# Optimization experiments

Measured on AMD Instinct MI355X. Metric: run time of the kernel, lower is better.

Reference implementation:

```python
import jax, jax.numpy as jnp
import numpy as np

B, N, E, H = 16, 577, 1024, 16          # batch, tokens (1 cls + 24x24 patches), embed, heads
HD = E // H
LORA_E, LORA_R = 4, 16                   # LoRA experts, rank
AD_E, AD_D = 4, 64                       # adapter experts, bottleneck
FF = 4 * E


def setup_inputs() -> dict:
    key = jax.random.key(0)
    ks = jax.random.split(key, 12)
    p = lambda i, shape: jax.random.normal(ks[i], shape, dtype=jnp.float32) * 0.02
    return {
        "tokens": jax.random.normal(ks[0], (B, N, E), dtype=jnp.float32),
        "ln1_g": jnp.ones((E,), jnp.float32), "ln1_b": jnp.zeros((E,), jnp.float32),
        "qkv_w": p(1, (3 * E, E)), "qkv_b": jnp.zeros((3 * E,), jnp.float32),
        "proj_w": p(2, (E, E)), "proj_b": jnp.zeros((E,), jnp.float32),
        "lora_gate_w": p(3, (LORA_E, E)),
        "lora_A": p(4, (LORA_E, LORA_R, E)),
        "lora_B": p(5, (LORA_E, 3 * E, LORA_R)),
        "ln2_g": jnp.ones((E,), jnp.float32), "ln2_b": jnp.zeros((E,), jnp.float32),
        "fc1_w": p(6, (FF, E)), "fc1_b": jnp.zeros((FF,), jnp.float32),
        "fc2_w": p(7, (E, FF)), "fc2_b": jnp.zeros((E,), jnp.float32),
        "ad_gate_w": p(8, (AD_E, E)),
        "ad_down_w": p(9, (AD_E, AD_D, E)), "ad_down_b": jnp.zeros((AD_E, AD_D), jnp.float32),
        "ad_up_w": p(10, (AD_E, E, AD_D)), "ad_up_b": jnp.zeros((AD_E, E), jnp.float32),
    }


def _ln(x, g, b):
    m = x.mean(-1, keepdims=True)
    v = ((x - m) ** 2).mean(-1, keepdims=True)
    return (x - m) * jax.lax.rsqrt(v + 1e-6) * g + b


def reference(tokens, ln1_g, ln1_b, qkv_w, qkv_b, proj_w, proj_b,
              lora_gate_w, lora_A, lora_B, ln2_g, ln2_b,
              fc1_w, fc1_b, fc2_w, fc2_b,
              ad_gate_w, ad_down_w, ad_down_b, ad_up_w, ad_up_b):
    # ---- attention with MoE-LoRA delta on fused QKV ----
    normed = _ln(tokens, ln1_g, ln1_b)                      # [B,N,E]
    qkv = normed @ qkv_w.T + qkv_b                          # [B,N,3E]
    gates = jax.nn.softmax(normed @ lora_gate_w.T, axis=-1)  # [B,N,X]
    h = jnp.einsum('bnd,xrd->bnxr', normed, lora_A)         # low-rank down
    delta = jnp.einsum('bnxr,bnx,xor->bno', h, gates, lora_B)  # gate-weighted up
    qkv = (qkv + delta).reshape(B, N, 3, H, HD).transpose(2, 0, 3, 1, 4)
    q, k, v = qkv[0], qkv[1], qkv[2]                        # [B,H,N,hd]
    scores = jnp.einsum('bhqd,bhkd->bhqk', q, k) * (HD ** -0.5)
    probs = jax.nn.softmax(scores, axis=-1)
    ctx = jnp.einsum('bhqk,bhkd->bhqd', probs, v)
    ctx = ctx.transpose(0, 2, 1, 3).reshape(B, N, E)
    tokens = tokens + (ctx @ proj_w.T + proj_b)
    # ---- MLP + MoE adapter branch (shared norm2 input) ----
    mlp_in = _ln(tokens, ln2_g, ln2_b)
    mlp_out = jax.nn.gelu(mlp_in @ fc1_w.T + fc1_b, approximate=False) @ fc2_w.T + fc2_b
    ag = jax.nn.softmax(mlp_in @ ad_gate_w.T, axis=-1)       # [B,N,Xa]
    ah = jax.nn.gelu(jnp.einsum('bnd,xhd->bnxh', mlp_in, ad_down_w) + ad_down_b,
                     approximate=False)
    ad_out = (jnp.einsum('bnxh,bnx,xoh->bno', ah, ag, ad_up_w)
              + jnp.einsum('bnx,xo->bno', ag, ad_up_b))
    return tokens + mlp_out + ad_out
```

## Files before the change

kernel.cpp:

```cpp
#include <hip/hip_runtime.h>
#include <math.h>

#define TOK 9232
#define EMB 1024
#define NQKV 3072
#define FFD 4096
#define NSEQ 577

typedef __bf16 bf16x8 __attribute__((ext_vector_type(8)));
typedef float f32x4 __attribute__((ext_vector_type(4)));
typedef unsigned short ushort8 __attribute__((ext_vector_type(8)));
typedef unsigned short ushort4v __attribute__((ext_vector_type(4)));

typedef __attribute__((address_space(3))) unsigned int lds_u32_t;
typedef const __attribute__((address_space(1))) unsigned int glob_u32_t;

__device__ __forceinline__ void async16(void* lds, const void* g) {
    __builtin_amdgcn_global_load_lds((glob_u32_t*)g, (lds_u32_t*)lds, 16, 0, 0);
}

__device__ __forceinline__ unsigned short f2bf(float f) {
    unsigned int u = __builtin_bit_cast(unsigned int, f);
    u = (u + 0x7fffu + ((u >> 16) & 1u)) >> 16;
    return (unsigned short)u;
}
__device__ __forceinline__ float bf2f(unsigned short s) {
    unsigned int u = ((unsigned int)s) << 16;
    return __builtin_bit_cast(float, u);
}
__device__ __forceinline__ float gelu_exact(float x) {
    return 0.5f * x * (1.0f + erff(x * 0.70710678118654752f));
}

__global__ void k_pack_all(const float* __restrict__ s_qkv, const float* __restrict__ s_proj,
                           const float* __restrict__ s_fc1, const float* __restrict__ s_fc2,
                           const float* __restrict__ s_la,  const float* __restrict__ s_ad,
                           unsigned short* __restrict__ d_qkv, unsigned short* __restrict__ d_proj,
                           unsigned short* __restrict__ d_fc1, unsigned short* __restrict__ d_fc2,
                           unsigned short* __restrict__ d_la,  unsigned short* __restrict__ d_ad) {
    int stride = gridDim.x * 256;
    for (int i4 = blockIdx.x * 256 + threadIdx.x; i4 < 3227648; i4 += stride) {
        const float* s; unsigned short* d; int local;
        if (i4 < 786432)       { s = s_qkv;  d = d_qkv;  local = i4; }
        else if (i4 < 1048576) { s = s_proj; d = d_proj; local = i4 - 786432; }
        else if (i4 < 2097152) { s = s_fc1;  d = d_fc1;  local = i4 - 1048576; }
        else if (i4 < 3145728) { s = s_fc2;  d = d_fc2;  local = i4 - 2097152; }
        else if (i4 < 3162112) { s = s_la;   d = d_la;   local = i4 - 3145728; }
        else                   { s = s_ad;   d = d_ad;   local = i4 - 3162112; }
        float4 v = ((const float4*)s)[local];
        ushort4v o;
        o[0] = f2bf(v.x); o[1] = f2bf(v.y); o[2] = f2bf(v.z); o[3] = f2bf(v.w);
        ((ushort4v*)d)[local] = o;
    }
}
__global__ void k_pack_bcat(const float* __restrict__ Bw, unsigned short* __restrict__ out) {
    int i = blockIdx.x * 256 + threadIdx.x;
    if (i >= 3072 * 64) return;
    int o = i >> 6, j = i & 63, x = j >> 4, r = j & 15;
    out[o * 64 + j] = f2bf(Bw[x * 3072 * 16 + o * 16 + r]);
}
__global__ void k_pack_u(const float* __restrict__ Uw, unsigned short* __restrict__ out) {
    int i = blockIdx.x * 256 + threadIdx.x;
    if (i >= 1024 * 256) return;
    int o = i >> 8, j = i & 255, x = j >> 6, h = j & 63;
    out[o * 256 + j] = f2bf(Uw[x * 65536 + o * 64 + h]);
}

template<bool FC2I>
__global__ __launch_bounds__(256) void k_ln_gates(const float* __restrict__ x,
                                                  const float* __restrict__ g,
                                                  const float* __restrict__ b,
                                                  const float* __restrict__ gw,
                                                  unsigned short* __restrict__ out,
                                                  float* __restrict__ gates,
                                                  const float* __restrict__ fc2b,
                                                  const float* __restrict__ upb,
                                                  float* __restrict__ out2) {
    int t = blockIdx.x;
    int tid = threadIdx.x;
    const float* xp = x + (size_t)t * EMB;
    float4 v = ((const float4*)xp)[tid];
    float s = v.x + v.y + v.z + v.w;
    float sq = v.x * v.x + v.y * v.y + v.z * v.z + v.w * v.w;
    #pragma unroll
    for (int off = 32; off > 0; off >>= 1) {
        s += __shfl_down(s, off);
        sq += __shfl_down(sq, off);
    }
    __shared__ float red[8];
    if ((tid & 63) == 0) { red[tid >> 6] = s; red[(tid >> 6) + 4] = sq; }
    __syncthreads();
    float S = red[0] + red[1] + red[2] + red[3];
    float SQ = red[4] + red[5] + red[6] + red[7];
    float mean = S * (1.0f / EMB);
    float var = SQ * (1.0f / EMB) - mean * mean;
    float rstd = rsqrtf(var + 1e-6f);
    float4 gv = ((const float4*)g)[tid];
    float4 bv = ((const float4*)b)[tid];
    float n0 = (v.x - mean) * rstd * gv.x + bv.x;
    float n1 = (v.y - mean) * rstd * gv.y + bv.y;
    float n2 = (v.z - mean) * rstd * gv.z + bv.z;
    float n3 = (v.w - mean) * rstd * gv.w + bv.w;
    ushort4v o;
    o[0] = f2bf(n0); o[1] = f2bf(n1); o[2] = f2bf(n2); o[3] = f2bf(n3);
    ((ushort4v*)(out + (size_t)t * EMB))[tid] = o;
    float p[4];
    #pragma unroll
    for (int xx = 0; xx < 4; ++xx) {
        float4 gr = ((const float4*)(gw + xx * EMB))[tid];
        p[xx] = n0 * gr.x + n1 * gr.y + n2 * gr.z + n3 * gr.w;
    }
    #pragma unroll
    for (int off = 32; off > 0; off >>= 1) {
        #pragma unroll
        for (int xx = 0; xx < 4; ++xx) p[xx] += __shfl_down(p[xx], off);
    }
    __shared__ float red2[4][4];
    __shared__ float agb[4];
    if ((tid & 63) == 0) {
        #pragma unroll
        for (int xx = 0; xx < 4; ++xx) red2[tid >> 6][xx] = p[xx];
    }
    __syncthreads();
    if (tid == 0) {
        float l[4];
        #pragma unroll
        for (int xx = 0; xx < 4; ++xx) l[xx] = red2[0][xx] + red2[1][xx] + red2[2][xx] + red2[3][xx];
        float m = fmaxf(fmaxf(l[0], l[1]), fmaxf(l[2], l[3]));
        float e[4], ssum = 0.f;
        #pragma unroll
        for (int xx = 0; xx < 4; ++xx) { e[xx] = expf(l[xx] - m); ssum += e[xx]; }
        float inv = 1.0f / ssum;
        #pragma unroll
        for (int xx = 0; xx < 4; ++xx) {
            float gg = e[xx] * inv;
            gates[t * 4 + xx] = gg;
            if (FC2I) agb[xx] = gg;
        }
    }
    if (FC2I) {
        __syncthreads();
        float g0 = agb[0], g1 = agb[1], g2 = agb[2], g3 = agb[3];
        float4 b0 = ((const float4*)(upb + 0 * EMB))[tid];
        float4 b1 = ((const float4*)(upb + 1 * EMB))[tid];
        float4 b2 = ((const float4*)(upb + 2 * EMB))[tid];
        float4 b3 = ((const float4*)(upb + 3 * EMB))[tid];
        float4 fb = ((const float4*)fc2b)[tid];
        float4 r;
        r.x = v.x + fb.x + g0 * b0.x + g1 * b1.x + g2 * b2.x + g3 * b3.x;
        r.y = v.y + fb.y + g0 * b0.y + g1 * b1.y + g2 * b2.y + g3 * b3.y;
        r.z = v.z + fb.z + g0 * b0.z + g1 * b1.z + g2 * b2.z + g3 * b3.z;
        r.w = v.w + fb.w + g0 * b0.w + g1 * b1.w + g2 * b2.w + g3 * b3.w;
        ((float4*)(out2 + (size_t)t * EMB))[tid] = r;
    }
}

#define BAR __builtin_amdgcn_s_barrier()

template<bool GELU, bool BF16OUT, int GG, int MF, int NF, int CN>
__global__ __launch_bounds__(256) void k_gemm(
    const unsigned short* __restrict__ A, int lda,
    const unsigned short* __restrict__ W, int ldw, int K1,
    int M, int N,
    const unsigned short* __restrict__ A2, const unsigned short* __restrict__ W2, int K2,
    const float* __restrict__ bias, const float* __restrict__ resid,
    const float* __restrict__ aux,
    void* __restrict__ Cout, int ldc, int gy)
{
    constexpr int CA = MF * 4;
    constexpr int CB = NF * 4;
    constexpr int CT = CA + CB;
    constexpr int CPW = CT / 4;
    constexpr int BUFB = CT * 1024;
    __shared__ __attribute__((aligned(16))) char Sbuf[2 * BUFB];

    int tid = threadIdx.x;
    int nwg = gridDim.x, orig = blockIdx.x;
    int xcd = orig & 7, lid = orig >> 3;
    int q = nwg >> 3, r = nwg & 7;
    int wg = (xcd < r ? xcd * (q + 1) : r * (q + 1) + (xcd - r) * q) + lid;
    int nmt = nwg / gy;
    int ni = wg % CN;
    int tmp = wg / CN;
    int mt = tmp % nmt;
    int nt = (tmp / nmt) * CN + ni;
    int bm = mt * (MF * 32);
    int bn = nt * (NF * 32);

    int l = tid & 63, w = tid >> 6;
    int wr = w >> 1, wc = w & 1;
    int lr = l & 15;
    int sslot = (((l & 7) ^ (l >> 3)) << 3);

    int KT1 = K1 >> 6, KT2 = K2 >> 6;
    int KT = KT1 + KT2;

    const unsigned short* A2s = A2 ? A2 : A;
    const unsigned short* W2s = W2 ? W2 : W;
    int K2s = A2 ? K2 : lda;

    const unsigned short* sp1[CPW];
    const unsigned short* sp2[CPW];
    int ldsu[CPW];
    #pragma unroll
    for (int j = 0; j < CPW; ++j) {
        int c = w * CPW + j;
        ldsu[j] = c << 10;
        if (c < CA) {
            int rw = bm + c * 8 + (l >> 3); if (rw > M - 1) rw = M - 1;
            sp1[j] = A + (size_t)rw * lda + sslot;
            sp2[j] = A2s + (size_t)rw * K2s + sslot;
        } else {
            int rw = bn + (c - CA) * 8 + (l >> 3); if (rw > N - 1) rw = N - 1;
            sp1[j] = W + (size_t)rw * ldw + sslot;
            sp2[j] = W2s + (size_t)rw * K2s + sslot;
        }
    }

    int offA[MF][2], offB[NF][2];
    #pragma unroll
    for (int m = 0; m < MF; ++m)
        #pragma unroll
        for (int ks = 0; ks < 2; ++ks) {
            int rw = wr * (MF * 16) + m * 16 + lr;
            int g = ks * 4 + (l >> 4);
            offA[m][ks] = (rw << 7) + ((g ^ (rw & 7)) << 4);
        }
    #pragma unroll
    for (int n = 0; n < NF; ++n)
        #pragma unroll
        for (int ks = 0; ks < 2; ++ks) {
            int rw = wc * (NF * 16) + n * 16 + lr;
            int g = ks * 4 + (l >> 4);
            offB[n][ks] = (CA << 10) + (rw << 7) + ((g ^ (rw & 7)) << 4);
        }

    f32x4 acc[MF][NF];
    #pragma unroll
    for (int m = 0; m < MF; ++m)
        #pragma unroll
        for (int n = 0; n < NF; ++n) acc[m][n] = (f32x4){0.f, 0.f, 0.f, 0.f};

    auto stage = [&](int ss, int bb) {
        char* db = Sbuf + bb * BUFB;
        if (ss < KT1) {
            int ko = ss << 6;
            #pragma unroll
            for (int j = 0; j < CPW; ++j) async16(db + ldsu[j], sp1[j] + ko);
        } else {
            int ko = (ss - KT1) << 6;
            #pragma unroll
            for (int j = 0; j < CPW; ++j) async16(db + ldsu[j], sp2[j] + ko);
        }
    };

    stage(0, 0);

    #pragma unroll 1
    for (int t = 0; t < KT; ++t) {
        asm volatile("s_waitcnt vmcnt(0)" ::: "memory");
        BAR;
        __builtin_amdgcn_sched_barrier(0);
        int s = t + 1; if (s >= KT) s = 0;
        stage(s, (t + 1) & 1);
        const char* base = Sbuf + (t & 1) * BUFB;
        bf16x8 af[MF][2], bfr[NF][2];
        #pragma unroll
        for (int m = 0; m < MF; ++m)
            #pragma unroll
            for (int ks = 0; ks < 2; ++ks) af[m][ks] = *(const bf16x8*)(base + offA[m][ks]);
        #pragma unroll
        for (int n = 0; n < NF; ++n)
            #pragma unroll
            for (int ks = 0; ks < 2; ++ks) bfr[n][ks] = *(const bf16x8*)(base + offB[n][ks]);
        __builtin_amdgcn_s_setprio(1);
        #pragma unroll
        for (int m = 0; m < MF; ++m)
            #pragma unroll
            for (int n = 0; n < NF; ++n)
                #pragma unroll
                for (int ks = 0; ks < 2; ++ks)
                    acc[m][n] = __builtin_amdgcn_mfma_f32_16x16x32_bf16(af[m][ks], bfr[n][ks], acc[m][n], 0, 0, 0);
        __builtin_amdgcn_s_setprio(0);
    }

    int rbase = bm + wr * (MF * 16);
    int cbase = bn + wc * (NF * 16);
    #pragma unroll
    for (int n = 0; n < NF; ++n) {
        int col = cbase + n * 16 + lr;
        if (col >= N) continue;
        float bv = bias ? bias[col] : 0.0f;
        #pragma unroll
        for (int m = 0; m < MF; ++m) {
            #pragma unroll
            for (int rr = 0; rr < 4; ++rr) {
                int row = rbase + m * 16 + (l >> 4) * 4 + rr;
                if (row >= M) continue;
                float c = acc[m][n][rr] + bv;
                if (GELU) c = gelu_exact(c);
                if (GG > 0) c *= aux[row * 4 + col / (GG > 0 ? GG : 1)];
                if (resid) c += resid[(size_t)row * ldc + col];
                if (BF16OUT) ((unsigned short*)Cout)[(size_t)row * ldc + col] = f2bf(c);
                else ((float*)Cout)[(size_t)row * ldc + col] = c;
            }
        }
    }
}

__global__ __launch_bounds__(256) void k_attn(const unsigned short* __restrict__ qkv,
                                              unsigned short* __restrict__ ctx) {
    int bh = blockIdx.x;
    int qt = blockIdx.y;
    int b = bh >> 4, h = bh & 15;
    int tid = threadIdx.x;
    int l = tid & 63;
    int w = tid >> 6;
    int lr = l & 15;
    int lk = (l >> 4) * 8;

    __shared__ unsigned short Qs[64][72];
    __shared__ unsigned short Ks[64][72];
    __shared__ unsigned short Vt[64][72];
    __shared__ unsigned short Ps[64][72];

    const size_t base = (size_t)b * NSEQ * NQKV + (size_t)h * 64;
    int q0 = qt * 64;

    {
        int row = tid >> 2, ds = (tid & 3) * 16;
        int qrow = q0 + row;
        if (qrow < NSEQ) {
            const unsigned short* src = qkv + base + (size_t)qrow * NQKV + ds;
            *(ushort8*)&Qs[row][ds] = *(const ushort8*)src;
            *(ushort8*)&Qs[row][ds + 8] = *(const ushort8*)(src + 8);
        } else {
            ushort8 z = {};
            *(ushort8*)&Qs[row][ds] = z;
            *(ushort8*)&Qs[row][ds + 8] = z;
        }
    }

    float m_run[4], l_run[4];
    f32x4 o[4];
    #pragma unroll
    for (int r = 0; r < 4; ++r) { m_run[r] = -1e30f; l_run[r] = 0.0f; }
    #pragma unroll
    for (int n = 0; n < 4; ++n) o[n] = (f32x4){0.f, 0.f, 0.f, 0.f};

    for (int kt = 0; kt < 10; ++kt) {
        __syncthreads();
        {
            int row = tid >> 2, ds = (tid & 3) * 16;
            int key = kt * 64 + row;
            if (key < NSEQ) {
                const unsigned short* ksrc = qkv + base + (size_t)key * NQKV + 1024 + ds;
                *(ushort8*)&Ks[row][ds] = *(const ushort8*)ksrc;
                *(ushort8*)&Ks[row][ds + 8] = *(const ushort8*)(ksrc + 8);
                const unsigned short* vsrc = qkv + base + (size_t)key * NQKV + 2048 + ds;
                #pragma unroll
                for (int j = 0; j < 16; ++j) Vt[ds + j][row] = vsrc[j];
            } else {
                ushort8 z = {};
                *(ushort8*)&Ks[row][ds] = z;
                *(ushort8*)&Ks[row][ds + 8] = z;
                #pragma unroll
                for (int j = 0; j < 16; ++j) Vt[ds + j][row] = 0;
            }
        }
        __syncthreads();

        f32x4 s[4];
        #pragma unroll
        for (int n = 0; n < 4; ++n) s[n] = (f32x4){0.f, 0.f, 0.f, 0.f};
        #pragma unroll
        for (int ks = 0; ks < 2; ++ks) {
            bf16x8 qa = *(const bf16x8*)&Qs[w * 16 + lr][ks * 32 + lk];
            #pragma unroll
            for (int n = 0; n < 4; ++n) {
                bf16x8 kb = *(const bf16x8*)&Ks[n * 16 + lr][ks * 32 + lk];
                s[n] = __builtin_amdgcn_mfma_f32_16x16x32_bf16(qa, kb, s[n], 0, 0, 0);
            }
        }
        #pragma unroll
        for (int n = 0; n < 4; ++n) {
            #pragma unroll
            for (int r = 0; r < 4; ++r) s[n][r] *= 0.125f;
        }
        #pragma unroll
        for (int n = 0; n < 4; ++n) {
            int col = kt * 64 + n * 16 + lr;
            if (col >= NSEQ) {
                #pragma unroll
                for (int r = 0; r < 4; ++r) s[n][r] = -1e30f;
            }
        }
        float tmax[4];
        #pragma unroll
        for (int r = 0; r < 4; ++r)
            tmax[r] = fmaxf(fmaxf(s[0][r], s[1][r]), fmaxf(s[2][r], s[3][r]));
        #pragma unroll
        for (int off = 1; off < 16; off <<= 1) {
            #pragma unroll
            for (int r = 0; r < 4; ++r) tmax[r] = fmaxf(tmax[r], __shfl_xor(tmax[r], off));
        }
        float alpha[4], rs[4];
        #pragma unroll
        for (int r = 0; r < 4; ++r) {
            float mn = fmaxf(m_run[r], tmax[r]);
            alpha[r] = __expf(m_run[r] - mn);
            m_run[r] = mn;
            rs[r] = 0.0f;
        }
        #pragma unroll
        for (int n = 0; n < 4; ++n) {
            #pragma unroll
            for (int r = 0; r < 4; ++r) {
                float p = __expf(s[n][r] - m_run[r]);
                s[n][r] = p;
                rs[r] += p;
            }
        }
        #pragma unroll
        for (int off = 1; off < 16; off <<= 1) {
            #pragma unroll
            for (int r = 0; r < 4; ++r) rs[r] += __shfl_xor(rs[r], off);
        }
        #pragma unroll
        for (int r = 0; r < 4; ++r) l_run[r] = l_run[r] * alpha[r] + rs[r];
        #pragma unroll
        for (int n = 0; n < 4; ++n) {
            #pragma unroll
            for (int r = 0; r < 4; ++r) o[n][r] *= alpha[r];
        }
        #pragma unroll
        for (int n = 0; n < 4; ++n) {
            #pragma unroll
            for (int r = 0; r < 4; ++r)
                Ps[w * 16 + (l >> 4) * 4 + r][n * 16 + lr] = f2bf(s[n][r]);
        }
        __syncthreads();
        #pragma unroll
        for (int ks = 0; ks < 2; ++ks) {
            bf16x8 pa = *(const bf16x8*)&Ps[w * 16 + lr][ks * 32 + lk];
            #pragma unroll
            for (int n = 0; n < 4; ++n) {
                bf16x8 vb = *(const bf16x8*)&Vt[n * 16 + lr][ks * 32 + lk];
                o[n] = __builtin_amdgcn_mfma_f32_16x16x32_bf16(pa, vb, o[n], 0, 0, 0);
            }
        }
    }
    #pragma unroll
    for (int r = 0; r < 4; ++r) {
        int qrow = q0 + w * 16 + (l >> 4) * 4 + r;
        if (qrow < NSEQ) {
            float inv = (l_run[r] > 0.f) ? 1.0f / l_run[r] : 0.0f;
            #pragma unroll
            for (int n = 0; n < 4; ++n)
                ctx[((size_t)b * NSEQ + qrow) * EMB + h * 64 + n * 16 + lr] = f2bf(o[n][r] * inv);
        }
    }
}

extern "C" void kernel_launch(void* const* d_in, const int* in_sizes, int n_in,
                              void* d_out, int out_size, void* d_ws, size_t ws_size,
                              hipStream_t stream) {
    const float* tokens      = (const float*)d_in[0];
    const float* ln1_g       = (const float*)d_in[1];
    const float* ln1_b       = (const float*)d_in[2];
    const float* qkv_w       = (const float*)d_in[3];
    const float* qkv_b       = (const float*)d_in[4];
    const float* proj_w      = (const float*)d_in[5];
    const float* proj_b      = (const float*)d_in[6];
    const float* lora_gate_w = (const float*)d_in[7];
    const float* lora_A      = (const float*)d_in[8];
    const float* lora_B      = (const float*)d_in[9];
    const float* ln2_g       = (const float*)d_in[10];
    const float* ln2_b       = (const float*)d_in[11];
    const float* fc1_w       = (const float*)d_in[12];
    const float* fc1_b       = (const float*)d_in[13];
    const float* fc2_w       = (const float*)d_in[14];
    const float* fc2_b       = (const float*)d_in[15];
    const float* ad_gate_w   = (const float*)d_in[16];
    const float* ad_down_w   = (const float*)d_in[17];
    const float* ad_down_b   = (const float*)d_in[18];
    const float* ad_up_w     = (const float*)d_in[19];
    const float* ad_up_b     = (const float*)d_in[20];

    char* ws = (char*)d_ws;
    size_t off = 0;
    auto alloc = [&](size_t bytes) -> void* {
        void* p = ws + off;
        off += (bytes + 255) & ~(size_t)255;
        return p;
    };

    unsigned short* w_qkv  = (unsigned short*)alloc((size_t)NQKV * EMB * 2);
    unsigned short* w_proj = (unsigned short*)alloc((size_t)EMB * EMB * 2);
    unsigned short* w_fc1  = (unsigned short*)alloc((size_t)FFD * EMB * 2);
    unsigned short* w_fc2  = (unsigned short*)alloc((size_t)EMB * FFD * 2);
    unsigned short* w_acat = (unsigned short*)alloc((size_t)64 * EMB * 2);
    unsigned short* w_bcat = (unsigned short*)alloc((size_t)NQKV * 64 * 2);
    unsigned short* w_dcat = (unsigned short*)alloc((size_t)256 * EMB * 2);
    unsigned short* w_u    = (unsigned short*)alloc((size_t)EMB * 256 * 2);

    unsigned short* u1 = (unsigned short*)alloc((size_t)TOK * EMB * 2);
    unsigned short* u2 = (unsigned short*)alloc((size_t)TOK * EMB * 2);
    unsigned short* u3 = (unsigned short*)alloc((size_t)TOK * FFD * 2);
    float* tok2  = (float*)alloc((size_t)TOK * EMB * 4);
    unsigned short* hw  = (unsigned short*)alloc((size_t)TOK * 64 * 2);
    unsigned short* ahw = (unsigned short*)alloc((size_t)TOK * 256 * 2);
    float* gates = (float*)alloc((size_t)TOK * 4 * 4);
    float* ag    = (float*)alloc((size_t)TOK * 4 * 4);

    unsigned short* normed = u1;
    unsigned short* mlpin  = u1;
    unsigned short* ctx    = u2;
    unsigned short* qkv    = u3;
    unsigned short* h1     = u3;

    k_pack_all<<<2048, 256, 0, stream>>>(qkv_w, proj_w, fc1_w, fc2_w, lora_A, ad_down_w,
                                         w_qkv, w_proj, w_fc1, w_fc2, w_acat, w_dcat);
    k_pack_bcat<<<(NQKV * 64 + 255) / 256, 256, 0, stream>>>(lora_B, w_bcat);
    k_pack_u<<<(EMB * 256 + 255) / 256, 256, 0, stream>>>(ad_up_w, w_u);

    k_ln_gates<false><<<TOK, 256, 0, stream>>>(tokens, ln1_g, ln1_b, lora_gate_w,
                                               normed, gates, nullptr, nullptr, nullptr);
    k_gemm<false, true, 16, 2, 2, 1><<<145, 256, 0, stream>>>(
        normed, EMB, w_acat, EMB, EMB, TOK, 64,
        nullptr, nullptr, 0, nullptr, nullptr, gates, hw, 64, 1);
    k_gemm<false, true, 0, 4, 2, 8><<<73 * 48, 256, 0, stream>>>(
        normed, EMB, w_qkv, EMB, EMB, TOK, NQKV,
        hw, w_bcat, 64, qkv_b, nullptr, nullptr, qkv, NQKV, 48);
    k_attn<<<dim3(256, 10), 256, 0, stream>>>(qkv, ctx);
    k_gemm<false, false, 0, 4, 2, 8><<<73 * 16, 256, 0, stream>>>(
        ctx, EMB, w_proj, EMB, EMB, TOK, EMB,
        nullptr, nullptr, 0, proj_b, tokens, nullptr, tok2, EMB, 16);
    k_ln_gates<true><<<TOK, 256, 0, stream>>>(tok2, ln2_g, ln2_b, ad_gate_w,
                                              mlpin, ag, fc2_b, ad_up_b, (float*)d_out);
    k_gemm<true, true, 64, 2, 2, 4><<<145 * 4, 256, 0, stream>>>(
        mlpin, EMB, w_dcat, EMB, EMB, TOK, 256,
        nullptr, nullptr, 0, ad_down_b, nullptr, ag, ahw, 256, 4);
    k_gemm<true, true, 0, 4, 2, 8><<<73 * 64, 256, 0, stream>>>(
        mlpin, EMB, w_fc1, EMB, EMB, TOK, FFD,
        nullptr, nullptr, 0, fc1_b, nullptr, nullptr, h1, FFD, 64);
    k_gemm<false, false, 0, 4, 2, 8><<<73 * 16, 256, 0, stream>>>(
        h1, FFD, w_fc2, FFD, FFD, TOK, EMB,
        ahw, w_u, 256, nullptr, (const float*)d_out, nullptr, (float*)d_out, EMB, 16);
}
```

Before: 634.9 us.

## Add 256x256-tile 8-wave pipelined GEMM kernel for fc1

Introduces a new GEMM kernel with 256x256 output tiles, 512 threads, an XOR-swizzled double-buffered LDS layout and an interleaved stage/MFMA schedule with explicit vmcnt waits and setprio. The fc1 projection now uses it instead of the 128x128-style generic kernel, aiming for more data reuse per loaded tile and better overlap of global loads with MFMA work. In exchange it needs large LDS and register use at occupancy 1, and wastes more padded rows in the last M tile since 9232 is not a multiple of 256.

```diff
diff --git a/kernel.cpp b/kernel.cpp
--- a/kernel.cpp
+++ b/kernel.cpp
@@ -303,6 +303,167 @@
                 if (resid) c += resid[(size_t)row * ldc + col];
                 if (BF16OUT) ((unsigned short*)Cout)[(size_t)row * ldc + col] = f2bf(c);
                 else ((float*)Cout)[(size_t)row * ldc + col] = c;
+            }
+        }
+    }
+}
+
+__device__ __forceinline__ void stage_half256(
+    const unsigned short* __restrict__ src, int ldk, int kc,
+    int row0, int rmax, char* lds_half, int w, int l)
+{
+    #pragma unroll
+    for (int j = 0; j < 2; ++j) {
+        int P = j * 8192 + w * 1024 + l * 16;
+        int row = P >> 7;
+        int slot = ((P >> 4) & 7) ^ (row & 7);
+        int r = row0 + row; if (r > rmax) r = rmax;
+        async16(lds_half + j * 8192 + w * 1024,
+                src + (size_t)r * ldk + kc + slot * 8);
+    }
+}
+
+__device__ __forceinline__ bf16x8 lds_frag256(const char* tile, int row, int c0) {
+    int byte = (row << 7) + (c0 << 1);
+    byte ^= (row & 7) << 4;
+    return *(const bf16x8*)(tile + byte);
+}
+
+#define STAGE256_A(s, ht, Pb) do {                                         \
+    int s_ = (s); if (s_ >= KT) s_ = 0;                                    \
+    stage_half256(A, K, s_ << 6, bm + (ht) * 128, M - 1,                   \
+                  (char*)SA + (Pb) * 32768 + (ht) * 16384, w, l);          \
+} while (0)
+
+#define STAGE256_B(s, ht, Pb) do {                                         \
+    int s_ = (s); if (s_ >= KT) s_ = 0;                                    \
+    stage_half256(W, K, s_ << 6, bn + (ht) * 128, N - 1,                   \
+                  (char*)SB + (Pb) * 32768 + (ht) * 16384, w, l);          \
+} while (0)
+
+#define LDA256(Pb, MH)                                                     \
+    _Pragma("unroll")                                                      \
+    for (int f_ = 0; f_ < 4; ++f_)                                         \
+        _Pragma("unroll")                                                  \
+        for (int ks_ = 0; ks_ < 2; ++ks_)                                  \
+            a[f_][ks_] = lds_frag256((const char*)SA + (Pb) * 32768,       \
+                wm * 128 + (MH) * 64 + f_ * 16 + lr, ks_ * 32 + lk8);
+
+#define LDB256(Pb, NH, BREG)                                               \
+    _Pragma("unroll")                                                      \
+    for (int n_ = 0; n_ < 2; ++n_)                                         \
+        _Pragma("unroll")                                                  \
+        for (int ks_ = 0; ks_ < 2; ++ks_)                                  \
+            BREG[n_][ks_] = lds_frag256((const char*)SB + (Pb) * 32768,    \
+                wn * 64 + (NH) * 32 + n_ * 16 + lr, ks_ * 32 + lk8);
+
+#define MFMA256(MH, NH, BREG)                                              \
+    __builtin_amdgcn_s_setprio(1);                                         \
+    _Pragma("unroll")                                                      \
+    for (int f_ = 0; f_ < 4; ++f_)                                         \
+        _Pragma("unroll")                                                  \
+        for (int n_ = 0; n_ < 2; ++n_)                                     \
+            _Pragma("unroll")                                              \
+            for (int ks_ = 0; ks_ < 2; ++ks_)                              \
+                acc[(MH) * 4 + f_][(NH) * 2 + n_] =                        \
+                    __builtin_amdgcn_mfma_f32_16x16x32_bf16(               \
+                        a[f_][ks_], BREG[n_][ks_],                         \
+                        acc[(MH) * 4 + f_][(NH) * 2 + n_], 0, 0, 0);       \
+    __builtin_amdgcn_s_setprio(0);
+
+#define VMCNT4_256 asm volatile("s_waitcnt vmcnt(4)" ::: "memory")
+
+template<bool GELU, bool BF16OUT>
+__global__ __launch_bounds__(512, 1) void k_gemm256(
+    const unsigned short* __restrict__ A, const unsigned short* __restrict__ W,
+    int M, int N, int K,
+    const float* __restrict__ bias,
+    void* __restrict__ Cout, int ldc, int NT)
+{
+    __shared__ __attribute__((aligned(16))) unsigned short SA[2][256][64];
+    __shared__ __attribute__((aligned(16))) unsigned short SB[2][256][64];
+
+    int tid = threadIdx.x;
+    int l = tid & 63, w = tid >> 6;
+    int wm = w >> 2, wn = w & 3;
+    int lr = l & 15, lk8 = (l >> 4) * 8;
+
+    int nwg = gridDim.x, orig = blockIdx.x;
+    int xcd = orig & 7, lid = orig >> 3;
+    int q = nwg >> 3, r = nwg & 7;
+    int wg = (xcd < r ? xcd * (q + 1) : r * (q + 1) + (xcd - r) * q) + lid;
+    int bm = (wg / NT) * 256;
+    int bn = (wg % NT) * 256;
+
+    int KT = K >> 6;
+
+    f32x4 acc[8][4];
+    #pragma unroll
+    for (int i = 0; i < 8; ++i)
+        #pragma unroll
+        for (int j = 0; j < 4; ++j) acc[i][j] = (f32x4){0.f, 0.f, 0.f, 0.f};
+
+    STAGE256_A(0, 0, 0); STAGE256_A(0, 1, 0);
+    STAGE256_B(0, 0, 0); STAGE256_B(0, 1, 0);
+    STAGE256_B(1, 0, 1); STAGE256_B(1, 1, 1);
+    VMCNT4_256;
+    BAR;
+
+    bf16x8 a[4][2], b0[2][2], b1[2][2];
+
+    int SI = KT >> 1;
+    #pragma unroll 1
+    for (int i = 0; i < SI; ++i) {
+        int t0 = i * 2;
+        LDA256(0, 0); LDB256(0, 0, b0);
+        STAGE256_A(t0 + 1, 0, 1);
+        BAR; MFMA256(0, 0, b0); BAR;
+
+        LDB256(0, 1, b1);
+        STAGE256_A(t0 + 1, 1, 1);
+        BAR; MFMA256(0, 1, b1); BAR;
+
+        LDA256(0, 1);
+        STAGE256_B(t0 + 2, 0, 0);
+        BAR; MFMA256(1, 0, b0); BAR;
+
+        STAGE256_B(t0 + 2, 1, 0);
+        VMCNT4_256;
+        BAR; MFMA256(1, 1, b1); BAR;
+
+        LDA256(1, 0); LDB256(1, 0, b0);
+        STAGE256_A(t0 + 2, 0, 0);
+        BAR; MFMA256(0, 0, b0); BAR;
+
+        LDB256(1, 1, b1);
+        STAGE256_A(t0 + 2, 1, 0);
+        BAR; MFMA256(0, 1, b1); BAR;
+
+        LDA256(1, 1);
+        STAGE256_B(t0 + 3, 0, 1);
+        BAR; MFMA256(1, 0, b0); BAR;
+
+        STAGE256_B(t0 + 3, 1, 1);
+        VMCNT4_256;
+        BAR; MFMA256(1, 1, b1); BAR;
+    }
+
+    #pragma unroll
+    for (int G = 0; G < 4; ++G) {
+        int col = bn + wn * 64 + (G >> 1) * 32 + (G & 1) * 16 + lr;
+        float bv = bias ? bias[col] : 0.0f;
+        #pragma unroll
+        for (int F = 0; F < 8; ++F) {
+            int row0 = bm + wm * 128 + (F >> 2) * 64 + (F & 3) * 16 + (l >> 4) * 4;
+            #pragma unroll
+            for (int rr = 0; rr < 4; ++rr) {
+                int row = row0 + rr;
+                if (row < M) {
+                    float c = acc[F][G][rr] + bv;
+                    if (GELU) c = gelu_exact(c);
+                    if (BF16OUT) ((unsigned short*)Cout)[(size_t)row * ldc + col] = f2bf(c);
+                    else ((float*)Cout)[(size_t)row * ldc + col] = c;
+                }
             }
         }
     }
@@ -541,9 +702,8 @@
     k_gemm<true, true, 64, 2, 2, 4><<<145 * 4, 256, 0, stream>>>(
         mlpin, EMB, w_dcat, EMB, EMB, TOK, 256,
         nullptr, nullptr, 0, ad_down_b, nullptr, ag, ahw, 256, 4);
-    k_gemm<true, true, 0, 4, 2, 8><<<73 * 64, 256, 0, stream>>>(
-        mlpin, EMB, w_fc1, EMB, EMB, TOK, FFD,
-        nullptr, nullptr, 0, fc1_b, nullptr, nullptr, h1, FFD, 64);
+    k_gemm256<true, true><<<37 * 16, 512, 0, stream>>>(
+        mlpin, w_fc1, TOK, FFD, EMB, fc1_b, h1, FFD, 16);
     k_gemm<false, false, 0, 4, 2, 8><<<73 * 16, 256, 0, stream>>>(
         h1, FFD, w_fc2, FFD, FFD, TOK, EMB,
         ahw, w_u, 256, nullptr, (const float*)d_out, nullptr, (float*)d_out, EMB, 16);
```

Measured after the change: 692.8 us. 1.09x slower.

## Halve GEMM K-step to 32 and widen N tiles to 128 columns

Applied to the files above, without the earlier changes.

The GEMM kernel's K-tile shrinks from 64 to 32 elements per stage, with a new LDS row layout and XOR swizzle sized for 64-byte rows. The freed shared memory goes to wider tiles: the big QKV, proj, fc1 and fc2 GEMMs move from 128x64 to 128x128 output tiles, which halves their grid sizes. The aim is more operand reuse per LDS load and fewer global fetches per FLOP. In exchange there are twice as many barrier-synchronised K iterations, each doing less MFMA work, so latency may be harder to hide. More accumulators per thread may also cut occupancy.

```diff
diff --git a/kernel.cpp b/kernel.cpp
--- a/kernel.cpp
+++ b/kernel.cpp
@@ -167,8 +167,8 @@
     const float* __restrict__ aux,
     void* __restrict__ Cout, int ldc, int gy)
 {
-    constexpr int CA = MF * 4;
-    constexpr int CB = NF * 4;
+    constexpr int CA = MF * 2;
+    constexpr int CB = NF * 2;
     constexpr int CT = CA + CB;
     constexpr int CPW = CT / 4;
     constexpr int BUFB = CT * 1024;
@@ -190,9 +190,9 @@
     int l = tid & 63, w = tid >> 6;
     int wr = w >> 1, wc = w & 1;
     int lr = l & 15;
-    int sslot = (((l & 7) ^ (l >> 3)) << 3);
-
-    int KT1 = K1 >> 6, KT2 = K2 >> 6;
+    int sslot = (((l & 3) ^ ((l >> 3) & 3)) << 3);
+
+    int KT1 = K1 >> 5, KT2 = K2 >> 5;
     int KT = KT1 + KT2;
 
     const unsigned short* A2s = A2 ? A2 : A;
@@ -207,33 +207,22 @@
         int c = w * CPW + j;
         ldsu[j] = c << 10;
         if (c < CA) {
-            int rw = bm + c * 8 + (l >> 3); if (rw > M - 1) rw = M - 1;
+            int rw = bm + c * 16 + (l >> 2); if (rw > M - 1) rw = M - 1;
             sp1[j] = A + (size_t)rw * lda + sslot;
             sp2[j] = A2s + (size_t)rw * K2s + sslot;
         } else {
-            int rw = bn + (c - CA) * 8 + (l >> 3); if (rw > N - 1) rw = N - 1;
+            int rw = bn + (c - CA) * 16 + (l >> 2); if (rw > N - 1) rw = N - 1;
             sp1[j] = W + (size_t)rw * ldw + sslot;
             sp2[j] = W2s + (size_t)rw * K2s + sslot;
         }
     }
 
-    int offA[MF][2], offB[NF][2];
-    #pragma unroll
-    for (int m = 0; m < MF; ++m)
-        #pragma unroll
-        for (int ks = 0; ks < 2; ++ks) {
-            int rw = wr * (MF * 16) + m * 16 + lr;
-            int g = ks * 4 + (l >> 4);
-            offA[m][ks] = (rw << 7) + ((g ^ (rw & 7)) << 4);
-        }
-    #pragma unroll
-    for (int n = 0; n < NF; ++n)
-        #pragma unroll
-        for (int ks = 0; ks < 2; ++ks) {
-            int rw = wc * (NF * 16) + n * 16 + lr;
-            int g = ks * 4 + (l >> 4);
-            offB[n][ks] = (CA << 10) + (rw << 7) + ((g ^ (rw & 7)) << 4);
-        }
+    int psl = ((l >> 4) ^ ((lr >> 1) & 3)) << 4;
+    int offA[MF], offB[NF];
+    #pragma unroll
+    for (int m = 0; m < MF; ++m) offA[m] = ((wr * (MF * 16) + m * 16 + lr) << 6) + psl;
+    #pragma unroll
+    for (int n = 0; n < NF; ++n) offB[n] = (CA << 10) + ((wc * (NF * 16) + n * 16 + lr) << 6) + psl;
 
     f32x4 acc[MF][NF];
     #pragma unroll
@@ -244,11 +233,11 @@
     auto stage = [&](int ss, int bb) {
         char* db = Sbuf + bb * BUFB;
         if (ss < KT1) {
-            int ko = ss << 6;
+            int ko = ss << 5;
             #pragma unroll
             for (int j = 0; j < CPW; ++j) async16(db + ldsu[j], sp1[j] + ko);
         } else {
-            int ko = (ss - KT1) << 6;
+            int ko = (ss - KT1) << 5;
             #pragma unroll
             for (int j = 0; j < CPW; ++j) async16(db + ldsu[j], sp2[j] + ko);
         }
@@ -264,23 +253,17 @@
         int s = t + 1; if (s >= KT) s = 0;
         stage(s, (t + 1) & 1);
         const char* base = Sbuf + (t & 1) * BUFB;
-        bf16x8 af[MF][2], bfr[NF][2];
+        bf16x8 af[MF], bfr[NF];
+        #pragma unroll
+        for (int m = 0; m < MF; ++m) af[m] = *(const bf16x8*)(base + offA[m]);
+        #pragma unroll
+        for (int n = 0; n < NF; ++n) bfr[n] = *(const bf16x8*)(base + offB[n]);
+        __builtin_amdgcn_s_setprio(1);
         #pragma unroll
         for (int m = 0; m < MF; ++m)
             #pragma unroll
-            for (int ks = 0; ks < 2; ++ks) af[m][ks] = *(const bf16x8*)(base + offA[m][ks]);
-        #pragma unroll
-        for (int n = 0; n < NF; ++n)
-            #pragma unroll
-            for (int ks = 0; ks < 2; ++ks) bfr[n][ks] = *(const bf16x8*)(base + offB[n][ks]);
-        __builtin_amdgcn_s_setprio(1);
-        #pragma unroll
-        for (int m = 0; m < MF; ++m)
-            #pragma unroll
             for (int n = 0; n < NF; ++n)
-                #pragma unroll
-                for (int ks = 0; ks < 2; ++ks)
-                    acc[m][n] = __builtin_amdgcn_mfma_f32_16x16x32_bf16(af[m][ks], bfr[n][ks], acc[m][n], 0, 0, 0);
+                acc[m][n] = __builtin_amdgcn_mfma_f32_16x16x32_bf16(af[m], bfr[n], acc[m][n], 0, 0, 0);
         __builtin_amdgcn_s_setprio(0);
     }
 
@@ -529,22 +512,22 @@
     k_gemm<false, true, 16, 2, 2, 1><<<145, 256, 0, stream>>>(
         normed, EMB, w_acat, EMB, EMB, TOK, 64,
         nullptr, nullptr, 0, nullptr, nullptr, gates, hw, 64, 1);
-    k_gemm<false, true, 0, 4, 2, 8><<<73 * 48, 256, 0, stream>>>(
+    k_gemm<false, true, 0, 4, 4, 8><<<73 * 24, 256, 0, stream>>>(
         normed, EMB, w_qkv, EMB, EMB, TOK, NQKV,
-        hw, w_bcat, 64, qkv_b, nullptr, nullptr, qkv, NQKV, 48);
+        hw, w_bcat, 64, qkv_b, nullptr, nullptr, qkv, NQKV, 24);
     k_attn<<<dim3(256, 10), 256, 0, stream>>>(qkv, ctx);
-    k_gemm<false, false, 0, 4, 2, 8><<<73 * 16, 256, 0, stream>>>(
+    k_gemm<false, false, 0, 4, 4, 8><<<73 * 8, 256, 0, stream>>>(
         ctx, EMB, w_proj, EMB, EMB, TOK, EMB,
-        nullptr, nullptr, 0, proj_b, tokens, nullptr, tok2, EMB, 16);
+        nullptr, nullptr, 0, proj_b, tokens, nullptr, tok2, EMB, 8);
     k_ln_gates<true><<<TOK, 256, 0, stream>>>(tok2, ln2_g, ln2_b, ad_gate_w,
                                               mlpin, ag, fc2_b, ad_up_b, (float*)d_out);
     k_gemm<true, true, 64, 2, 2, 4><<<145 * 4, 256, 0, stream>>>(
         mlpin, EMB, w_dcat, EMB, EMB, TOK, 256,
         nullptr, nullptr, 0, ad_down_b, nullptr, ag, ahw, 256, 4);
-    k_gemm<true, true, 0, 4, 2, 8><<<73 * 64, 256, 0, stream>>>(
+    k_gemm<true, true, 0, 4, 4, 8><<<73 * 32, 256, 0, stream>>>(
         mlpin, EMB, w_fc1, EMB, EMB, TOK, FFD,
-        nullptr, nullptr, 0, fc1_b, nullptr, nullptr, h1, FFD, 64);
-    k_gemm<false, false, 0, 4, 2, 8><<<73 * 16, 256, 0, stream>>>(
+        nullptr, nullptr, 0, fc1_b, nullptr, nullptr, h1, FFD, 32);
+    k_gemm<false, false, 0, 4, 4, 8><<<73 * 8, 256, 0, stream>>>(
         h1, FFD, w_fc2, FFD, FFD, TOK, EMB,
-        ahw, w_u, 256, nullptr, (const float*)d_out, nullptr, (float*)d_out, EMB, 16);
-}
+        ahw, w_u, 256, nullptr, (const float*)d_out, nullptr, (float*)d_out, EMB, 8);
+}
```

Measured after the change: 677.0 us. +6.6%, slower.
